# Optimization experiments

Measured on AMD Instinct MI355X. Metric: run time of the kernel, lower is better.

## Reference

```python
import jax, jax.numpy as jnp
import numpy as np
from math import sqrt

B, L, S = 4, 2048, 2048
D_MODEL, H = 1024, 16
E = D_MODEL // H  # head dim = 64


def setup_inputs() -> dict:
    key = jax.random.key(0)
    ks = jax.random.split(key, 11)
    s = 1.0 / sqrt(D_MODEL)
    return {
        "queries": jax.random.normal(ks[0], (B, L, D_MODEL), jnp.float32),
        "keys": jax.random.normal(ks[1], (B, S, D_MODEL), jnp.float32),
        "values": jax.random.normal(ks[2], (B, S, D_MODEL), jnp.float32),
        "Wq": jax.random.normal(ks[3], (D_MODEL, D_MODEL), jnp.float32) * s,
        "bq": jax.random.normal(ks[4], (D_MODEL,), jnp.float32) * s,
        "Wk": jax.random.normal(ks[5], (D_MODEL, D_MODEL), jnp.float32) * s,
        "bk": jax.random.normal(ks[6], (D_MODEL,), jnp.float32) * s,
        "Wv": jax.random.normal(ks[7], (D_MODEL, D_MODEL), jnp.float32) * s,
        "bv": jax.random.normal(ks[8], (D_MODEL,), jnp.float32) * s,
        "Wo": jax.random.normal(ks[9], (D_MODEL, D_MODEL), jnp.float32) * s,
        "bo": jax.random.normal(ks[10], (D_MODEL,), jnp.float32) * s,
    }


def reference(queries, keys, values, Wq, bq, Wk, bk, Wv, bv, Wo, bo):
    # QKV projections, split heads: [B, L/S, H, E]
    q = (queries @ Wq + bq).reshape(B, L, H, E)
    k = (keys @ Wk + bk).reshape(B, S, H, E)
    v = (values @ Wv + bv).reshape(B, S, H, E)
    scale = 1.0 / sqrt(E)
    scores = jnp.einsum('blhe,bshe->bhls', q, k)  # [B,H,L,S]
    A = jax.nn.softmax(scale * scores, axis=-1)   # dropout is identity in eval
    out = jnp.einsum('bhls,bshd->blhd', A, v).reshape(B, L, H * E)
    return out @ Wo + bo
```

## Files before the change

kernel.cpp:

```cpp
#include <hip/hip_runtime.h>
#include <hip/hip_bf16.h>

typedef unsigned short u16;
typedef unsigned int u32;
using short8 = __attribute__((ext_vector_type(8))) short;
using f32x4  = __attribute__((ext_vector_type(4))) float;
using f32x16 = __attribute__((ext_vector_type(16))) float;
using u32x2  = __attribute__((ext_vector_type(2))) unsigned int;
using u32x4  = __attribute__((ext_vector_type(4))) unsigned int;

#define B_  4
#define L_  2048
#define S_  2048
#define DM  1024
#define H_  16
#define E_  64

__device__ __forceinline__ u16 f2bf(float f) {
  union { float f; unsigned u; } v; v.f = f;
  unsigned u = v.u;
  unsigned r = (u + 0x7fffu + ((u >> 16) & 1u)) >> 16;
  return (u16)r;
}

__device__ __forceinline__ float exp2a(float x) {
  float r; asm("v_exp_f32 %0, %1" : "=v"(r) : "v"(x)); return r;
}

__device__ __forceinline__ u32 cvtpk(float lo, float hi) {
  u32 r; asm("v_cvt_pk_bf16_f32 %0, %1, %2" : "=v"(r) : "v"(lo), "v"(hi));
  return r;
}

__device__ __forceinline__ f32x4 mfma16(short8 a, short8 b, f32x4 c) {
  return __builtin_amdgcn_mfma_f32_16x16x32_bf16(a, b, c, 0, 0, 0);
}

__device__ __forceinline__ f32x16 mfma32(short8 a, short8 b, f32x16 c) {
  return __builtin_amdgcn_mfma_f32_32x32x16_bf16(a, b, c, 0, 0, 0);
}

__device__ __forceinline__ void gload_lds16(const u16* g, u16* l) {
  __builtin_amdgcn_global_load_lds(
      (const __attribute__((address_space(1))) unsigned int*)(const void*)g,
      (__attribute__((address_space(3))) unsigned int*)(void*)l, 16, 0, 0);
}

__global__ __launch_bounds__(256) void cvt_all(const float* __restrict__ s0,
                                               const float* __restrict__ s1,
                                               const float* __restrict__ s2,
                                               u16* __restrict__ d0,
                                               u16* __restrict__ d1,
                                               u16* __restrict__ d2) {
  const float* s = blockIdx.y == 0 ? s0 : blockIdx.y == 1 ? s1 : s2;
  u16* d = blockIdx.y == 0 ? d0 : blockIdx.y == 1 ? d1 : d2;
  int i = (blockIdx.x * 256 + threadIdx.x) * 4;
  f32x4 v = *(const f32x4*)(s + i);
  u32x2 o;
  o.x = cvtpk(v.x, v.y);
  o.y = cvtpk(v.z, v.w);
  *(u32x2*)(d + i) = o;
}

__global__ __launch_bounds__(256) void transp_all(const float* __restrict__ w0,
                                                  const float* __restrict__ w1,
                                                  const float* __restrict__ w2,
                                                  const float* __restrict__ w3,
                                                  u16* __restrict__ t0,
                                                  u16* __restrict__ t1,
                                                  u16* __restrict__ t2,
                                                  u16* __restrict__ t3) {
  const float* W = blockIdx.z == 0 ? w0 : blockIdx.z == 1 ? w1 :
                   blockIdx.z == 2 ? w2 : w3;
  u16* Wt = blockIdx.z == 0 ? t0 : blockIdx.z == 1 ? t1 :
            blockIdx.z == 2 ? t2 : t3;
  __shared__ float t[32][33];
  int tx = threadIdx.x & 31, ty = (threadIdx.x >> 5) & 7;
#pragma unroll
  for (int j = 0; j < 32; j += 8)
    t[ty + j][tx] = W[(size_t)(blockIdx.y * 32 + ty + j) * DM + blockIdx.x * 32 + tx];
  __syncthreads();
#pragma unroll
  for (int j = 0; j < 32; j += 8)
    Wt[(size_t)(blockIdx.x * 32 + ty + j) * DM + blockIdx.y * 32 + tx] = f2bf(t[tx][ty + j]);
}

template <int EPI>
__device__ __forceinline__ void gemm_body(const u16* __restrict__ A,
                                          const u16* __restrict__ Bt,
                                          const float* __restrict__ bias,
                                          void* __restrict__ Cout,
                                          int M, int N, int K, float oscale,
                                          int bx, int by) {
  __shared__ u16 lA[128 * 32];
  __shared__ u16 lB[128 * 32];
  const int tid = threadIdx.x, wid = tid >> 6, lane = tid & 63;
  const int lr = lane & 15, lh = lane >> 4;
  const int m0 = by * 128, n0 = bx * 128;
  const int wr = wid >> 1, wc = wid & 1;

  f32x4 acc[4][4];
#pragma unroll
  for (int m = 0; m < 4; m++)
#pragma unroll
    for (int n = 0; n < 4; n++) acc[m][n] = (f32x4){0.f, 0.f, 0.f, 0.f};

  const int srow = wid * 16 + (lane >> 2);
  const int scol = (lane & 3) * 8;

  for (int k0 = 0; k0 < K; k0 += 32) {
#pragma unroll
    for (int p = 0; p < 2; p++) {
      int r = p * 64 + srow;
      gload_lds16(A + (size_t)(m0 + r) * K + k0 + scol, lA + (p * 64 + wid * 16) * 32);
      gload_lds16(Bt + (size_t)(n0 + r) * K + k0 + scol, lB + (p * 64 + wid * 16) * 32);
    }
    __syncthreads();
    short8 af[4], bf[4];
#pragma unroll
    for (int m = 0; m < 4; m++)
      af[m] = *(const short8*)(lA + (wr * 64 + m * 16 + lr) * 32 + lh * 8);
#pragma unroll
    for (int n = 0; n < 4; n++)
      bf[n] = *(const short8*)(lB + (wc * 64 + n * 16 + lr) * 32 + lh * 8);
#pragma unroll
    for (int m = 0; m < 4; m++)
#pragma unroll
      for (int n = 0; n < 4; n++) acc[m][n] = mfma16(af[m], bf[n], acc[m][n]);
    __syncthreads();
  }

#pragma unroll
  for (int m = 0; m < 4; m++) {
    int grow0 = m0 + wr * 64 + m * 16 + lh * 4;
#pragma unroll
    for (int n = 0; n < 4; n++) {
      int gcol = n0 + wc * 64 + n * 16 + lr;
      float bi = bias[gcol];
      float v0 = (acc[m][n][0] + bi) * oscale;
      float v1 = (acc[m][n][1] + bi) * oscale;
      float v2 = (acc[m][n][2] + bi) * oscale;
      float v3 = (acc[m][n][3] + bi) * oscale;
      if constexpr (EPI == 2) {
        float* C = (float*)Cout;
        C[(size_t)(grow0 + 0) * N + gcol] = v0;
        C[(size_t)(grow0 + 1) * N + gcol] = v1;
        C[(size_t)(grow0 + 2) * N + gcol] = v2;
        C[(size_t)(grow0 + 3) * N + gcol] = v3;
      } else {
        u32 p01 = cvtpk(v0, v1), p23 = cvtpk(v2, v3);
        u16* C = (u16*)Cout;
#pragma unroll
        for (int r = 0; r < 4; r++) {
          u32 pk = r < 2 ? p01 : p23;
          u16 bv = (r & 1) ? (u16)(pk >> 16) : (u16)(pk & 0xffff);
          int grow = grow0 + r;
          if constexpr (EPI == 0) {
            C[(size_t)grow * N + gcol] = bv;
          } else {
            int bb = grow >> 11, sl = grow & 2047;
            C[((size_t)(bb * DM) + gcol) * S_ + sl] = bv;
          }
        }
      }
    }
  }
}

__global__ __launch_bounds__(256) void gemm_qkv(
    const u16* __restrict__ qb, const u16* __restrict__ kb, const u16* __restrict__ vb,
    const u16* __restrict__ WqT, const u16* __restrict__ WkT, const u16* __restrict__ WvT,
    const float* __restrict__ bq, const float* __restrict__ bk, const float* __restrict__ bv,
    u16* __restrict__ Qp, u16* __restrict__ Kp, u16* __restrict__ Vt, float qsc) {
  const int z = blockIdx.z;
  if (z == 0)
    gemm_body<0>(qb, WqT, bq, Qp, B_ * L_, DM, DM, qsc, blockIdx.x, blockIdx.y);
  else if (z == 1)
    gemm_body<0>(kb, WkT, bk, Kp, B_ * L_, DM, DM, 1.0f, blockIdx.x, blockIdx.y);
  else
    gemm_body<1>(vb, WvT, bv, Vt, B_ * L_, DM, DM, 1.0f, blockIdx.x, blockIdx.y);
}

__global__ __launch_bounds__(256) void gemm_out(const u16* __restrict__ A,
                                                const u16* __restrict__ Bt,
                                                const float* __restrict__ bias,
                                                float* __restrict__ C) {
  gemm_body<2>(A, Bt, bias, C, B_ * L_, DM, DM, 1.0f, blockIdx.x, blockIdx.y);
}

__global__ __launch_bounds__(512) void attn(const u16* __restrict__ Q,
                                            const u16* __restrict__ Kp,
                                            const u16* __restrict__ Vt,
                                            u16* __restrict__ O) {
  __shared__ u16 lK[2][64 * 64];
  __shared__ u16 lV[2][64 * 64];
  const int tid = threadIdx.x, wid = tid >> 6, lane = tid & 63;
  const int l31 = lane & 31, hi = lane >> 5;

  int lin = blockIdx.x;
  int swz = (lin & 7) * 64 + (lin >> 3);
  const int bh = swz >> 3, q0 = (swz & 7) * 256;
  const int b = bh >> 4, h = bh & 15;
  const int qrow = q0 + wid * 32 + l31;

  const u16* Qb = Q + ((size_t)(b * L_ + qrow)) * DM + h * E_ + hi * 8;
  short8 qf[4];
#pragma unroll
  for (int s = 0; s < 4; s++) qf[s] = *(const short8*)(Qb + s * 16);

  f32x16 o[2];
#pragma unroll
  for (int et = 0; et < 2; et++)
#pragma unroll
    for (int r = 0; r < 16; r++) o[et][r] = 0.f;
  float m_r = -3.0e38f, l_r = 0.f;

  const u16* Kb = Kp + ((size_t)(b * S_)) * DM + h * E_;
  const u16* Vb = Vt + ((size_t)(b * DM + h * E_)) * S_;

  const int srow = wid * 8 + (lane >> 3);
  const u16* srcK = Kb + (size_t)srow * DM + ((lane & 7) ^ (srow & 7)) * 8;
  const u16* srcV = Vb + (size_t)srow * S_ + ((lane & 7) ^ (srow & 7)) * 8;

  const int sxk = (l31 & 7) * 8;
  const int hi4 = hi * 4, hi8 = hi * 8;

  auto stage = [&](int buf, int kb) {
    gload_lds16(srcK + (size_t)kb * DM, lK[buf] + wid * 512);
    gload_lds16(srcV + kb, lV[buf] + wid * 512);
  };

  stage(0, 0);
  const int NT = S_ / 64;
  for (int it = 0; it < NT; ++it) {
    const int buf = it & 1;
    __syncthreads();
    if (it + 1 < NT) stage(buf ^ 1, (it + 1) * 64);

    f32x16 sc[2];
    const u16* kbase = lK[buf] + l31 * 64;
    __builtin_amdgcn_s_setprio(1);
#pragma unroll
    for (int kt = 0; kt < 2; kt++) {
      f32x16 a;
#pragma unroll
      for (int r = 0; r < 16; r++) a[r] = 0.f;
#pragma unroll
      for (int s = 0; s < 4; s++) {
        short8 kf = *(const short8*)(kbase + kt * 2048 + ((s * 16 + hi8) ^ sxk));
        a = mfma32(kf, qf[s], a);
      }
      sc[kt] = a;
    }
    __builtin_amdgcn_s_setprio(0);

    f32x16 mA;
#pragma unroll
    for (int r = 0; r < 16; r++) mA[r] = fmaxf(sc[0][r], sc[1][r]);
#pragma unroll
    for (int r = 0; r < 8; r++) mA[r] = fmaxf(mA[r], mA[r + 8]);
#pragma unroll
    for (int r = 0; r < 4; r++) mA[r] = fmaxf(mA[r], mA[r + 4]);
    float tm = fmaxf(fmaxf(mA[0], mA[1]), fmaxf(mA[2], mA[3]));
    tm = fmaxf(tm, __shfl_xor(tm, 32));

    if (__any(tm > m_r + 8.f)) {
      float mn = fmaxf(m_r, tm);
      float al = exp2a(m_r - mn);
      m_r = mn;
      l_r *= al;
#pragma unroll
      for (int et = 0; et < 2; et++)
#pragma unroll
        for (int r = 0; r < 16; r++) o[et][r] *= al;
    }

    u32 wp[2][8];
    float rs = 0.f;
#pragma unroll
    for (int kt = 0; kt < 2; kt++)
#pragma unroll
      for (int i = 0; i < 8; i++) {
        float p0 = exp2a(sc[kt][2 * i] - m_r);
        float p1 = exp2a(sc[kt][2 * i + 1] - m_r);
        rs += p0 + p1;
        wp[kt][i] = cvtpk(p0, p1);
      }
    rs += __shfl_xor(rs, 32);
    l_r += rs;

    __builtin_amdgcn_s_setprio(1);
#pragma unroll
    for (int et = 0; et < 2; et++) {
      const u16* vp = lV[buf] + (et * 32 + l31) * 64;
#pragma unroll
      for (int kt = 0; kt < 2; kt++)
#pragma unroll
        for (int su = 0; su < 2; su++) {
          int koff = kt * 32 + su * 16 + hi4;
          u32x2 lo = *(const u32x2*)(vp + (koff ^ sxk));
          u32x2 hp = *(const u32x2*)(vp + ((koff + 8) ^ sxk));
          u32x4 vv = {lo.x, lo.y, hp.x, hp.y};
          u32x4 pv = {wp[kt][su * 4 + 0], wp[kt][su * 4 + 1],
                      wp[kt][su * 4 + 2], wp[kt][su * 4 + 3]};
          o[et] = mfma32(*(const short8*)&vv, *(const short8*)&pv, o[et]);
        }
    }
    __builtin_amdgcn_s_setprio(0);
  }

  float inv = 1.f / l_r;
  u16* Ob = O + ((size_t)(b * L_ + qrow)) * DM + h * E_;
#pragma unroll
  for (int et = 0; et < 2; et++)
#pragma unroll
    for (int t = 0; t < 4; t++) {
      u32x2 pk;
      pk.x = cvtpk(o[et][4 * t] * inv, o[et][4 * t + 1] * inv);
      pk.y = cvtpk(o[et][4 * t + 2] * inv, o[et][4 * t + 3] * inv);
      *(u32x2*)(Ob + et * 32 + t * 8 + hi4) = pk;
    }
}

extern "C" void kernel_launch(void* const* d_in, const int* in_sizes, int n_in,
                              void* d_out, int out_size, void* d_ws, size_t ws_size,
                              hipStream_t stream) {
  (void)in_sizes; (void)n_in; (void)out_size; (void)ws_size;
  const float* q  = (const float*)d_in[0];
  const float* k  = (const float*)d_in[1];
  const float* v  = (const float*)d_in[2];
  const float* Wq = (const float*)d_in[3];
  const float* bq = (const float*)d_in[4];
  const float* Wk = (const float*)d_in[5];
  const float* bk = (const float*)d_in[6];
  const float* Wv = (const float*)d_in[7];
  const float* bv = (const float*)d_in[8];
  const float* Wo = (const float*)d_in[9];
  const float* bo = (const float*)d_in[10];

  char* w = (char*)d_ws;
  const size_t ACT = (size_t)B_ * L_ * DM * 2;
  const size_t WT  = (size_t)DM * DM * 2;
  u16* qb  = (u16*)w; w += ACT;
  u16* kb  = (u16*)w; w += ACT;
  u16* vb  = (u16*)w; w += ACT;
  u16* WqT = (u16*)w; w += WT;
  u16* WkT = (u16*)w; w += WT;
  u16* WvT = (u16*)w; w += WT;
  u16* WoT = (u16*)w; w += WT;
  u16* Qp  = (u16*)w; w += ACT;
  u16* Kp  = (u16*)w; w += ACT;
  u16* Vt  = (u16*)w; w += ACT;
  u16* At  = (u16*)w; w += ACT;

  const int M = B_ * L_;
  cvt_all<<<dim3(M * DM / (4 * 256), 3), 256, 0, stream>>>(q, k, v, qb, kb, vb);
  transp_all<<<dim3(32, 32, 4), 256, 0, stream>>>(Wq, Wk, Wv, Wo, WqT, WkT, WvT, WoT);

  const float QSC = 0.125f * 1.44269504089f;
  gemm_qkv<<<dim3(DM / 128, M / 128, 3), 256, 0, stream>>>(
      qb, kb, vb, WqT, WkT, WvT, bq, bk, bv, Qp, Kp, Vt, QSC);

  attn<<<dim3(512), 512, 0, stream>>>(Qp, Kp, Vt, At);

  gemm_out<<<dim3(DM / 128, M / 128), 256, 0, stream>>>(At, WoT, bo, (float*)d_out);
}
```

Before: 232.8 us.

## Fold max subtraction into score MFMA init and compute row sums via MFMA

The score accumulator is now initialised to the negative running max, so each exp2 reads the score directly without a separate subtract. The row-sum of probabilities is computed by an extra MFMA against a ones vector instead of scalar adds plus a cross-lane shuffle. The max reduction is rewritten as a three-input fmax tree, and exponentiation is interleaved per key-tile with the PV MFMAs. This trims VALU work in the softmax at the cost of one extra MFMA per sub-step and a rescale of the scores whenever the running max is updated.

```diff
diff --git a/kernel.cpp b/kernel.cpp
--- a/kernel.cpp
+++ b/kernel.cpp
@@ -208,12 +208,13 @@
 #pragma unroll
   for (int s = 0; s < 4; s++) qf[s] = *(const short8*)(Qb + s * 16);
 
-  f32x16 o[2];
-#pragma unroll
-  for (int et = 0; et < 2; et++)
-#pragma unroll
-    for (int r = 0; r < 16; r++) o[et][r] = 0.f;
-  float m_r = -3.0e38f, l_r = 0.f;
+  u32x4 onesw = {0x3F803F80u, 0x3F803F80u, 0x3F803F80u, 0x3F803F80u};
+  short8 ones = *(const short8*)&onesw;
+
+  f32x16 o0, o1, lac;
+#pragma unroll
+  for (int r = 0; r < 16; r++) { o0[r] = 0.f; o1[r] = 0.f; lac[r] = 0.f; }
+  float m_r = 0.f;
 
   const u16* Kb = Kp + ((size_t)(b * S_)) * DM + h * E_;
   const u16* Vb = Vt + ((size_t)(b * DM + h * E_)) * S_;
@@ -239,12 +240,13 @@
 
     f32x16 sc[2];
     const u16* kbase = lK[buf] + l31 * 64;
+    const float negm = -m_r;
     __builtin_amdgcn_s_setprio(1);
 #pragma unroll
     for (int kt = 0; kt < 2; kt++) {
       f32x16 a;
 #pragma unroll
-      for (int r = 0; r < 16; r++) a[r] = 0.f;
+      for (int r = 0; r < 16; r++) a[r] = negm;
 #pragma unroll
       for (int s = 0; s < 4; s++) {
         short8 kf = *(const short8*)(kbase + kt * 2048 + ((s * 16 + hi8) ^ sxk));
@@ -254,72 +256,79 @@
     }
     __builtin_amdgcn_s_setprio(0);
 
-    f32x16 mA;
-#pragma unroll
-    for (int r = 0; r < 16; r++) mA[r] = fmaxf(sc[0][r], sc[1][r]);
-#pragma unroll
-    for (int r = 0; r < 8; r++) mA[r] = fmaxf(mA[r], mA[r + 8]);
-#pragma unroll
-    for (int r = 0; r < 4; r++) mA[r] = fmaxf(mA[r], mA[r + 4]);
-    float tm = fmaxf(fmaxf(mA[0], mA[1]), fmaxf(mA[2], mA[3]));
+    float t0 = fmaxf(fmaxf(sc[0][0], sc[0][1]), sc[0][2]);
+    float t1 = fmaxf(fmaxf(sc[0][3], sc[0][4]), sc[0][5]);
+    float t2 = fmaxf(fmaxf(sc[0][6], sc[0][7]), sc[0][8]);
+    float t3 = fmaxf(fmaxf(sc[0][9], sc[0][10]), sc[0][11]);
+    float t4 = fmaxf(fmaxf(sc[0][12], sc[0][13]), sc[0][14]);
+    float t5 = fmaxf(fmaxf(sc[0][15], sc[1][0]), sc[1][1]);
+    float t6 = fmaxf(fmaxf(sc[1][2], sc[1][3]), sc[1][4]);
+    float t7 = fmaxf(fmaxf(sc[1][5], sc[1][6]), sc[1][7]);
+    float t8 = fmaxf(fmaxf(sc[1][8], sc[1][9]), sc[1][10]);
+    float t9 = fmaxf(fmaxf(sc[1][11], sc[1][12]), sc[1][13]);
+    float ta = fmaxf(sc[1][14], sc[1][15]);
+    t0 = fmaxf(fmaxf(t0, t1), t2);
+    t3 = fmaxf(fmaxf(t3, t4), t5);
+    t6 = fmaxf(fmaxf(t6, t7), t8);
+    t9 = fmaxf(t9, ta);
+    float tm = fmaxf(fmaxf(t0, t3), fmaxf(t6, t9));
     tm = fmaxf(tm, __shfl_xor(tm, 32));
 
-    if (__any(tm > m_r + 8.f)) {
-      float mn = fmaxf(m_r, tm);
-      float al = exp2a(m_r - mn);
-      m_r = mn;
-      l_r *= al;
-#pragma unroll
-      for (int et = 0; et < 2; et++)
-#pragma unroll
-        for (int r = 0; r < 16; r++) o[et][r] *= al;
-    }
-
-    u32 wp[2][8];
-    float rs = 0.f;
-#pragma unroll
-    for (int kt = 0; kt < 2; kt++)
-#pragma unroll
-      for (int i = 0; i < 8; i++) {
-        float p0 = exp2a(sc[kt][2 * i] - m_r);
-        float p1 = exp2a(sc[kt][2 * i + 1] - m_r);
-        rs += p0 + p1;
-        wp[kt][i] = cvtpk(p0, p1);
+    if (__any(tm > 8.f)) {
+      float delta = fmaxf(tm, 0.f);
+      float al = exp2a(-delta);
+      m_r += delta;
+      lac[0] *= al;
+#pragma unroll
+      for (int r = 0; r < 16; r++) { o0[r] *= al; o1[r] *= al; }
+#pragma unroll
+      for (int kt = 0; kt < 2; kt++)
+#pragma unroll
+        for (int r = 0; r < 16; r++) sc[kt][r] -= delta;
+    }
+
+    const u16* vbase = lV[buf] + l31 * 64;
+    const u16* vbase1 = vbase + 2048;
+#pragma unroll
+    for (int kt = 0; kt < 2; kt++) {
+      u32 wpk[8];
+#pragma unroll
+      for (int i = 0; i < 8; i++)
+        wpk[i] = cvtpk(exp2a(sc[kt][2 * i]), exp2a(sc[kt][2 * i + 1]));
+      __builtin_amdgcn_s_setprio(1);
+#pragma unroll
+      for (int su = 0; su < 2; su++) {
+        u32x4 pw = {wpk[su * 4 + 0], wpk[su * 4 + 1],
+                    wpk[su * 4 + 2], wpk[su * 4 + 3]};
+        short8 pf = *(const short8*)&pw;
+        int ka = ((kt * 32 + su * 16 + hi4) ^ sxk);
+        int kb2 = ((kt * 32 + su * 16 + hi4 + 8) ^ sxk);
+        u32x2 lo0 = *(const u32x2*)(vbase + ka);
+        u32x2 hp0 = *(const u32x2*)(vbase + kb2);
+        u32x4 vv0 = {lo0.x, lo0.y, hp0.x, hp0.y};
+        o0 = mfma32(*(const short8*)&vv0, pf, o0);
+        u32x2 lo1 = *(const u32x2*)(vbase1 + ka);
+        u32x2 hp1 = *(const u32x2*)(vbase1 + kb2);
+        u32x4 vv1 = {lo1.x, lo1.y, hp1.x, hp1.y};
+        o1 = mfma32(*(const short8*)&vv1, pf, o1);
+        lac = mfma32(ones, pf, lac);
       }
-    rs += __shfl_xor(rs, 32);
-    l_r += rs;
-
-    __builtin_amdgcn_s_setprio(1);
-#pragma unroll
-    for (int et = 0; et < 2; et++) {
-      const u16* vp = lV[buf] + (et * 32 + l31) * 64;
-#pragma unroll
-      for (int kt = 0; kt < 2; kt++)
-#pragma unroll
-        for (int su = 0; su < 2; su++) {
-          int koff = kt * 32 + su * 16 + hi4;
-          u32x2 lo = *(const u32x2*)(vp + (koff ^ sxk));
-          u32x2 hp = *(const u32x2*)(vp + ((koff + 8) ^ sxk));
-          u32x4 vv = {lo.x, lo.y, hp.x, hp.y};
-          u32x4 pv = {wp[kt][su * 4 + 0], wp[kt][su * 4 + 1],
-                      wp[kt][su * 4 + 2], wp[kt][su * 4 + 3]};
-          o[et] = mfma32(*(const short8*)&vv, *(const short8*)&pv, o[et]);
-        }
-    }
-    __builtin_amdgcn_s_setprio(0);
+      __builtin_amdgcn_s_setprio(0);
+    }
   }
 
-  float inv = 1.f / l_r;
+  float inv = 1.f / lac[0];
   u16* Ob = O + ((size_t)(b * L_ + qrow)) * DM + h * E_;
 #pragma unroll
-  for (int et = 0; et < 2; et++)
-#pragma unroll
-    for (int t = 0; t < 4; t++) {
-      u32x2 pk;
-      pk.x = cvtpk(o[et][4 * t] * inv, o[et][4 * t + 1] * inv);
-      pk.y = cvtpk(o[et][4 * t + 2] * inv, o[et][4 * t + 3] * inv);
-      *(u32x2*)(Ob + et * 32 + t * 8 + hi4) = pk;
-    }
+  for (int t = 0; t < 4; t++) {
+    u32x2 pk;
+    pk.x = cvtpk(o0[4 * t] * inv, o0[4 * t + 1] * inv);
+    pk.y = cvtpk(o0[4 * t + 2] * inv, o0[4 * t + 3] * inv);
+    *(u32x2*)(Ob + t * 8 + hi4) = pk;
+    pk.x = cvtpk(o1[4 * t] * inv, o1[4 * t + 1] * inv);
+    pk.y = cvtpk(o1[4 * t + 2] * inv, o1[4 * t + 3] * inv);
+    *(u32x2*)(Ob + 32 + t * 8 + hi4) = pk;
+  }
 }
 
 extern "C" void kernel_launch(void* const* d_in, const int* in_sizes, int n_in,
```

After: 241.6 us. 1.04x slower.

## Fuse fp32-to-bf16 activation conversion into QKV GEMM loads and swizzle block order

Applied to the files above, without the earlier changes.

Drops the separate conversion kernel that wrote bf16 copies of the query, key and value inputs. The QKV GEMM now reads fp32 activations directly, converts them in registers and stores them to LDS, which saves an extra round trip through global memory. Both GEMMs switch to a 1D grid with an XCD-aware swizzle, and the output GEMM gets its own bf16 body with an fp32 epilogue. In exchange, A-operand loads become synchronous register loads instead of direct-to-LDS, and each tile is reloaded and reconverted across the N-blocks.

```diff
diff --git a/kernel.cpp b/kernel.cpp
--- a/kernel.cpp
+++ b/kernel.cpp
@@ -44,22 +44,6 @@
   __builtin_amdgcn_global_load_lds(
       (const __attribute__((address_space(1))) unsigned int*)(const void*)g,
       (__attribute__((address_space(3))) unsigned int*)(void*)l, 16, 0, 0);
-}
-
-__global__ __launch_bounds__(256) void cvt_all(const float* __restrict__ s0,
-                                               const float* __restrict__ s1,
-                                               const float* __restrict__ s2,
-                                               u16* __restrict__ d0,
-                                               u16* __restrict__ d1,
-                                               u16* __restrict__ d2) {
-  const float* s = blockIdx.y == 0 ? s0 : blockIdx.y == 1 ? s1 : s2;
-  u16* d = blockIdx.y == 0 ? d0 : blockIdx.y == 1 ? d1 : d2;
-  int i = (blockIdx.x * 256 + threadIdx.x) * 4;
-  f32x4 v = *(const f32x4*)(s + i);
-  u32x2 o;
-  o.x = cvtpk(v.x, v.y);
-  o.y = cvtpk(v.z, v.w);
-  *(u32x2*)(d + i) = o;
 }
 
 __global__ __launch_bounds__(256) void transp_all(const float* __restrict__ w0,
@@ -86,7 +70,7 @@
 }
 
 template <int EPI>
-__device__ __forceinline__ void gemm_body(const u16* __restrict__ A,
+__device__ __forceinline__ void gemm_body(const float* __restrict__ A,
                                           const u16* __restrict__ Bt,
                                           const float* __restrict__ bias,
                                           void* __restrict__ Cout,
@@ -112,7 +96,12 @@
 #pragma unroll
     for (int p = 0; p < 2; p++) {
       int r = p * 64 + srow;
-      gload_lds16(A + (size_t)(m0 + r) * K + k0 + scol, lA + (p * 64 + wid * 16) * 32);
+      const float* src = A + (size_t)(m0 + r) * K + k0 + scol;
+      f32x4 a0 = *(const f32x4*)src;
+      f32x4 a1 = *(const f32x4*)(src + 4);
+      u32x4 wv = {cvtpk(a0.x, a0.y), cvtpk(a0.z, a0.w),
+                  cvtpk(a1.x, a1.y), cvtpk(a1.z, a1.w)};
+      *(u32x4*)(lA + (size_t)r * 32 + scol) = wv;
       gload_lds16(Bt + (size_t)(n0 + r) * K + k0 + scol, lB + (p * 64 + wid * 16) * 32);
     }
     __syncthreads();
@@ -167,25 +156,88 @@
   }
 }
 
+__device__ __forceinline__ void gemm_body_bf16(const u16* __restrict__ A,
+                                               const u16* __restrict__ Bt,
+                                               const float* __restrict__ bias,
+                                               float* __restrict__ Cout,
+                                               int M, int N, int K,
+                                               int bx, int by) {
+  __shared__ u16 lA[128 * 32];
+  __shared__ u16 lB[128 * 32];
+  const int tid = threadIdx.x, wid = tid >> 6, lane = tid & 63;
+  const int lr = lane & 15, lh = lane >> 4;
+  const int m0 = by * 128, n0 = bx * 128;
+  const int wr = wid >> 1, wc = wid & 1;
+
+  f32x4 acc[4][4];
+#pragma unroll
+  for (int m = 0; m < 4; m++)
+#pragma unroll
+    for (int n = 0; n < 4; n++) acc[m][n] = (f32x4){0.f, 0.f, 0.f, 0.f};
+
+  const int srow = wid * 16 + (lane >> 2);
+  const int scol = (lane & 3) * 8;
+
+  for (int k0 = 0; k0 < K; k0 += 32) {
+#pragma unroll
+    for (int p = 0; p < 2; p++) {
+      int r = p * 64 + srow;
+      gload_lds16(A + (size_t)(m0 + r) * K + k0 + scol, lA + (p * 64 + wid * 16) * 32);
+      gload_lds16(Bt + (size_t)(n0 + r) * K + k0 + scol, lB + (p * 64 + wid * 16) * 32);
+    }
+    __syncthreads();
+    short8 af[4], bf[4];
+#pragma unroll
+    for (int m = 0; m < 4; m++)
+      af[m] = *(const short8*)(lA + (wr * 64 + m * 16 + lr) * 32 + lh * 8);
+#pragma unroll
+    for (int n = 0; n < 4; n++)
+      bf[n] = *(const short8*)(lB + (wc * 64 + n * 16 + lr) * 32 + lh * 8);
+#pragma unroll
+    for (int m = 0; m < 4; m++)
+#pragma unroll
+      for (int n = 0; n < 4; n++) acc[m][n] = mfma16(af[m], bf[n], acc[m][n]);
+    __syncthreads();
+  }
+
+#pragma unroll
+  for (int m = 0; m < 4; m++) {
+    int grow0 = m0 + wr * 64 + m * 16 + lh * 4;
+#pragma unroll
+    for (int n = 0; n < 4; n++) {
+      int gcol = n0 + wc * 64 + n * 16 + lr;
+      float bi = bias[gcol];
+#pragma unroll
+      for (int r = 0; r < 4; r++)
+        Cout[(size_t)(grow0 + r) * N + gcol] = acc[m][n][r] + bi;
+    }
+  }
+}
+
 __global__ __launch_bounds__(256) void gemm_qkv(
-    const u16* __restrict__ qb, const u16* __restrict__ kb, const u16* __restrict__ vb,
+    const float* __restrict__ q, const float* __restrict__ k, const float* __restrict__ v,
     const u16* __restrict__ WqT, const u16* __restrict__ WkT, const u16* __restrict__ WvT,
     const float* __restrict__ bq, const float* __restrict__ bk, const float* __restrict__ bv,
     u16* __restrict__ Qp, u16* __restrict__ Kp, u16* __restrict__ Vt, float qsc) {
-  const int z = blockIdx.z;
+  int lin = blockIdx.x;
+  int swz = (lin & 7) * 192 + (lin >> 3);
+  const int bx = swz & 7, by = (swz >> 3) & 63, z = swz >> 9;
   if (z == 0)
-    gemm_body<0>(qb, WqT, bq, Qp, B_ * L_, DM, DM, qsc, blockIdx.x, blockIdx.y);
+    gemm_body<0>(q, WqT, bq, Qp, B_ * L_, DM, DM, qsc, bx, by);
   else if (z == 1)
-    gemm_body<0>(kb, WkT, bk, Kp, B_ * L_, DM, DM, 1.0f, blockIdx.x, blockIdx.y);
+    gemm_body<0>(k, WkT, bk, Kp, B_ * L_, DM, DM, 1.0f, bx, by);
   else
-    gemm_body<1>(vb, WvT, bv, Vt, B_ * L_, DM, DM, 1.0f, blockIdx.x, blockIdx.y);
+    gemm_body<1>(v, WvT, bv, Vt, B_ * L_, DM, DM, 1.0f, bx, by);
 }
 
 __global__ __launch_bounds__(256) void gemm_out(const u16* __restrict__ A,
                                                 const u16* __restrict__ Bt,
                                                 const float* __restrict__ bias,
                                                 float* __restrict__ C) {
-  gemm_body<2>(A, Bt, bias, C, B_ * L_, DM, DM, 1.0f, blockIdx.x, blockIdx.y);
+  int lin = blockIdx.x;
+  int swz = (lin & 7) * 64 + (lin >> 3);
+  const int bx = swz & 7, by = swz >> 3;
+  gemm_body_bf16(A, Bt, bias, C, B_ * L_, DM, DM, bx, by);
 }
 
 __global__ __launch_bounds__(512) void attn(const u16* __restrict__ Q,
@@ -341,9 +393,6 @@
   char* w = (char*)d_ws;
   const size_t ACT = (size_t)B_ * L_ * DM * 2;
   const size_t WT  = (size_t)DM * DM * 2;
-  u16* qb  = (u16*)w; w += ACT;
-  u16* kb  = (u16*)w; w += ACT;
-  u16* vb  = (u16*)w; w += ACT;
   u16* WqT = (u16*)w; w += WT;
   u16* WkT = (u16*)w; w += WT;
   u16* WvT = (u16*)w; w += WT;
@@ -353,15 +402,13 @@
   u16* Vt  = (u16*)w; w += ACT;
   u16* At  = (u16*)w; w += ACT;
 
-  const int M = B_ * L_;
-  cvt_all<<<dim3(M * DM / (4 * 256), 3), 256, 0, stream>>>(q, k, v, qb, kb, vb);
   transp_all<<<dim3(32, 32, 4), 256, 0, stream>>>(Wq, Wk, Wv, Wo, WqT, WkT, WvT, WoT);
 
   const float QSC = 0.125f * 1.44269504089f;
-  gemm_qkv<<<dim3(DM / 128, M / 128, 3), 256, 0, stream>>>(
-      qb, kb, vb, WqT, WkT, WvT, bq, bk, bv, Qp, Kp, Vt, QSC);
+  gemm_qkv<<<dim3(1536), 256, 0, stream>>>(
+      q, k, v, WqT, WkT, WvT, bq, bk, bv, Qp, Kp, Vt, QSC);
 
   attn<<<dim3(512), 512, 0, stream>>>(Qp, Kp, Vt, At);
 
-  gemm_out<<<dim3(DM / 128, M / 128), 256, 0, stream>>>(At, WoT, bo, (float*)d_out);
-}
+  gemm_out<<<dim3(512), 256, 0, stream>>>(At, WoT, bo, (float*)d_out);
+}
```

Measured after the change: 222.1 us. 4.6% less time.
